# Kernel optimization log

Measured on AMD Instinct MI355X. Metric: run time of the kernel, lower is better.

Reference implementation:

```python
import jax, jax.numpy as jnp
import numpy as np

EPS = 1e-5
ABIT = 8
WBIT = 8


def ste_round(x):
    # straight-through rounding (HAWQ SymmetricQuantFunction)
    return x + jax.lax.stop_gradient(jnp.round(x) - x)


def quant_act(x, bit=ABIT):
    # per-tensor symmetric activation quantization (QuantAct)
    n = 2.0 ** (bit - 1) - 1  # 127
    scale = jnp.max(jnp.abs(x)) / n
    x_int = jnp.clip(ste_round(x / scale), -n - 1, n)
    return x_int * scale, scale


def setup_inputs() -> dict:
    key = jax.random.key(0)
    k = jax.random.split(key, 6)
    B, C_in, H, W, C_out = 32, 512, 32, 32, 128
    x = jax.random.normal(k[0], (B, C_in, H, W), jnp.float32)
    # incoming activation scale (input assumed already 8-bit quantized)
    act_scaling_factor = (jnp.max(jnp.abs(x)) / 127.0).reshape(1)
    bn_gamma = jax.random.uniform(k[1], (C_in,), jnp.float32, 0.5, 1.5)
    bn_beta = jax.random.normal(k[2], (C_in,), jnp.float32) * 0.1
    bn_mean = jax.random.normal(k[3], (C_in,), jnp.float32) * 0.1
    bn_var = jax.random.uniform(k[4], (C_in,), jnp.float32, 0.5, 1.5)
    conv_weight = jax.random.normal(k[5], (C_out, C_in, 3, 3), jnp.float32) / np.sqrt(C_in * 9)
    return {"x": x, "act_scaling_factor": act_scaling_factor,
            "bn_gamma": bn_gamma, "bn_beta": bn_beta,
            "bn_mean": bn_mean, "bn_var": bn_var,
            "conv_weight": conv_weight}


def reference(x, act_scaling_factor, bn_gamma, bn_beta, bn_mean, bn_var, conv_weight):
    nw = 2.0 ** (WBIT - 1) - 1  # 127
    s_in = act_scaling_factor.reshape(())

    # ---- QuantBn: fold BN into per-channel affine, quantize weight/bias ----
    w_bn = bn_gamma / jnp.sqrt(bn_var + EPS)            # [C_in]
    b_bn = bn_beta - bn_mean * w_bn                      # [C_in]
    ws_bn = jnp.max(jnp.abs(w_bn)) / nw                  # per-tensor weight scale
    w_int = jnp.clip(ste_round(w_bn / ws_bn), -nw - 1, nw)
    bn_sf = ws_bn * s_in                                 # bn output scaling factor
    b_int = ste_round(b_bn / bn_sf)
    x_int = x / s_in
    x = (x_int * w_int[None, :, None, None] + b_int[None, :, None, None]) * bn_sf

    # ---- ReLU ----
    x = jax.nn.relu(x)

    # ---- QuantAct: requantize activations to 8 bit ----
    x, s_act = quant_act(x)

    # ---- QuantConv2d: per-output-channel 8-bit weight quant, int conv ----
    ws_c = jnp.max(jnp.abs(conv_weight), axis=(1, 2, 3)) / nw       # [C_out]
    w_cint = jnp.clip(ste_round(conv_weight / ws_c[:, None, None, None]), -nw - 1, nw)
    y_int = jax.lax.conv_general_dilated(
        x / s_act, w_cint, window_strides=(1, 1), padding=((1, 1), (1, 1)),
        dimension_numbers=("NCHW", "OIHW", "NCHW"))
    conv_sf = s_act * ws_c                               # [C_out]
    y = y_int * conv_sf[None, :, None, None]

    # ---- QuantAct output requant ----
    y, s_out = quant_act(y)
    return (y, s_out)
```

## Files before the change

kernel.cpp:

```cpp
#include <hip/hip_runtime.h>


typedef int v4i __attribute__((ext_vector_type(4)));

#define WS_A1    64
#define WS_B1    2112
#define WS_WSC   4160
#define WS_XMX   4672
#define WS_XMN   6720
#define WS_WQ    8768
#define WS_X2    598592
#define WS_ZROW  18424384

__device__ __forceinline__ float wave_max(float m) {
#pragma unroll
    for (int off = 32; off; off >>= 1) m = fmaxf(m, __shfl_xor(m, off));
    return m;
}

__global__ __launch_bounds__(512) void k_prep(
    const float* __restrict__ gamma, const float* __restrict__ beta,
    const float* __restrict__ mean,  const float* __restrict__ var,
    const float* __restrict__ asf,   const float* __restrict__ cw,
    const float4* __restrict__ x4,
    float* ws_f, unsigned* ws_u, float* __restrict__ wsc,
    signed char* __restrict__ wq) {
    int t = threadIdx.x;
    int bid = blockIdx.x;
    __shared__ float red[16];
    if (bid < 512) {
        int c = bid;
        float mx = -3.4e38f, mn = 3.4e38f;
#pragma unroll
        for (int r = 0; r < 16; ++r) {
            int bbb = r * 2 + (t >> 8);
            float4 v = x4[((size_t)(bbb * 512 + c)) * 256 + (t & 255)];
            mx = fmaxf(mx, fmaxf(fmaxf(v.x, v.y), fmaxf(v.z, v.w)));
            mn = fminf(mn, fminf(fminf(v.x, v.y), fminf(v.z, v.w)));
        }
        mx = wave_max(mx);
        mn = -wave_max(-mn);
        if ((t & 63) == 0) { red[t >> 6] = mx; red[8 + (t >> 6)] = mn; }
        __syncthreads();
        if (t == 0) {
            float M = red[0], N = red[8];
#pragma unroll
            for (int i = 1; i < 8; ++i) { M = fmaxf(M, red[i]); N = fminf(N, red[8 + i]); }
            ws_f[WS_XMX / 4 + c] = M;
            ws_f[WS_XMN / 4 + c] = N;
        }
    } else if (bid < 640) {
        int co = bid - 512;
        const float* w = cw + (size_t)co * 4608;
        float m = 0.f;
        for (int j = t; j < 4608; j += 512) m = fmaxf(m, fabsf(w[j]));
        m = wave_max(m);
        if ((t & 63) == 0) red[t >> 6] = m;
        __syncthreads();
        float mall = red[0];
#pragma unroll
        for (int i = 1; i < 8; ++i) mall = fmaxf(mall, red[i]);
        float sc = mall / 127.0f;
        if (t == 0) wsc[co] = sc;
        int ci = t >> 6, cq = (t >> 4) & 3, cb = t & 15;
#pragma unroll
        for (int tap = 0; tap < 9; ++tap) {
            float q = fminf(fmaxf(rintf(w[t * 9 + tap] / sc), -128.f), 127.f);
            wq[(((size_t)(tap * 8 + ci) * 4 + cq) * 128 + co) * 16 + cb] = (signed char)q;
        }
    } else {
        float wbn = gamma[t] / sqrtf(var[t] + 1e-5f);
        float bbn = beta[t] - mean[t] * wbn;
        float m = wave_max(fabsf(wbn));
        if ((t & 63) == 0) red[t >> 6] = m;
        __syncthreads();
        float mall = red[0];
#pragma unroll
        for (int i = 1; i < 8; ++i) mall = fmaxf(mall, red[i]);
        float ws_bn = mall / 127.0f;
        float s_in  = asf[0];
        float bn_sf = ws_bn * s_in;
        float wint  = fminf(fmaxf(rintf(wbn / ws_bn), -128.f), 127.f);
        float bint  = rintf(bbn / bn_sf);
        ws_f[WS_A1 / 4 + t] = wint * bn_sf / s_in;
        ws_f[WS_B1 / 4 + t] = bint * bn_sf;
        if (t == 0) ws_u[1] = 0u;
    }
}

__global__ __launch_bounds__(256) void k_xquant(
    const float4* __restrict__ x4, float* __restrict__ ws_f,
    unsigned* __restrict__ x2u, unsigned* __restrict__ zrowu) {
    int bb = 31 - (blockIdx.x >> 5), h = blockIdx.x & 31;
    const float* A1 = ws_f + WS_A1 / 4;
    const float* B1 = ws_f + WS_B1 / 4;
    const float* XMX = ws_f + WS_XMX / 4;
    const float* XMN = ws_f + WS_XMN / 4;
    int t = threadIdx.x;

    __shared__ float sred[4];
    float cand = 0.f;
#pragma unroll
    for (int c0 = 0; c0 < 512; c0 += 256) {
        int c = c0 + t;
        float A = A1[c], B = B1[c];
        cand = fmaxf(cand, fmaxf(fmaf(XMX[c], A, B), fmaf(XMN[c], A, B)));
    }
    cand = wave_max(cand);
    if ((t & 63) == 0) sred[t >> 6] = cand;
    __syncthreads();
    float xm = fmaxf(fmaxf(sred[0], sred[1]), fmaxf(sred[2], sred[3]));
    float inv_sact = 127.0f / xm;
    if (blockIdx.x == 0 && t == 0) ws_f[3] = xm / 127.0f;

    size_t rowd = (size_t)(bb * 32 + h) * 4352;
    {
        int p = t >> 3, side = (t >> 2) & 1, d = t & 3;
        x2u[rowd + (p * 34 + side * 33) * 4 + d] = 0u;
    }
    if (blockIdx.x < 17) {
        int idx = blockIdx.x * 256 + t;
        if (idx < 4352) zrowu[idx] = 0u;
    }

    __shared__ unsigned lds[512 * 9];

#pragma unroll
    for (int it = 0; it < 16; ++it) {
        int idx = it * 256 + t;
        int c = idx >> 3, f4 = idx & 7;
        float4 v = x4[((size_t)bb * 512 + c) * 256 + h * 8 + f4];
        float A = A1[c] * inv_sact, B = B1[c] * inv_sact;
        unsigned q0 = (unsigned)(int)fminf(rintf(fmaxf(fmaf(v.x, A, B), 0.f)), 127.f);
        unsigned q1 = (unsigned)(int)fminf(rintf(fmaxf(fmaf(v.y, A, B), 0.f)), 127.f);
        unsigned q2 = (unsigned)(int)fminf(rintf(fmaxf(fmaf(v.z, A, B), 0.f)), 127.f);
        unsigned q3 = (unsigned)(int)fminf(rintf(fmaxf(fmaf(v.w, A, B), 0.f)), 127.f);
        lds[c * 9 + f4] = q0 | (q1 << 8) | (q2 << 16) | (q3 << 24);
    }
    __syncthreads();

#pragma unroll
    for (int it = 0; it < 4; ++it) {
        int p = it * 8 + (t >> 5);
        int s = (t >> 2) & 7;
        int k = t & 3;
        unsigned L[16];
#pragma unroll
        for (int j = 0; j < 16; ++j) L[j] = lds[(p * 16 + j) * 9 + s];
        uint4 o;
        unsigned* op = (unsigned*)&o;
#pragma unroll
        for (int d = 0; d < 4; ++d)
            op[d] = ((L[4 * d] >> (8 * k)) & 255u) |
                    (((L[4 * d + 1] >> (8 * k)) & 255u) << 8) |
                    (((L[4 * d + 2] >> (8 * k)) & 255u) << 16) |
                    (((L[4 * d + 3] >> (8 * k)) & 255u) << 24);
        *(uint4*)(x2u + rowd + (size_t)(p * 34 + s * 4 + 1 + k) * 4) = o;
    }
}

__global__ __launch_bounds__(256, 3) void k_conv(
    const unsigned char* __restrict__ x2, const unsigned char* __restrict__ zrow,
    const signed char* __restrict__ wq,
    const float* __restrict__ wsc, const float* __restrict__ ws_f,
    unsigned* __restrict__ amaxy, float* __restrict__ y) {
    __shared__ v4i red[2][1024];
    int t = threadIdx.x;
    int lane = t & 63, kv = t >> 6;
    int m = lane & 15, quad = lane >> 4;

    int bid = blockIdx.x;
    int tile = (bid & 7) * 128 + (bid >> 3);
    int ch = tile & 1;
    int rowpair = (tile >> 1) & 15;
    int bb = tile >> 5;
    int h0 = rowpair * 2;
    int co0 = ch * 64;

    const unsigned char* xb = x2 + (size_t)bb * (32 * 17408);
    const v4i* rp[4];
#pragma unroll
    for (int j = 0; j < 4; ++j) {
        int row = h0 - 1 + j;
        rp[j] = (const v4i*)(((unsigned)row < 32u) ? (xb + (size_t)row * 17408) : zrow);
    }

    v4i acc[4][4];
#pragma unroll
    for (int i = 0; i < 4; ++i)
#pragma unroll
        for (int j = 0; j < 4; ++j) acc[i][j] = (v4i){0, 0, 0, 0};

    const v4i* pw = (const v4i*)wq + quad * 128 + co0 + m;
    int abase = quad * 34 + m;

#pragma unroll
    for (int kh = 0; kh < 3; ++kh)
#pragma unroll
        for (int kw = 0; kw < 3; ++kw) {
            int tap = kh * 3 + kw;
#pragma unroll
            for (int cc = 0; cc < 2; ++cc) {
                int ci = kv * 2 + cc;
                v4i a[4];
#pragma unroll
                for (int mt = 0; mt < 4; ++mt)
                    a[mt] = rp[kh + (mt >> 1)][ci * 136 + abase + kw + (mt & 1) * 16];
#pragma unroll
                for (int nt = 0; nt < 4; ++nt) {
                    v4i bf = pw[(tap * 8 + ci) * 512 + nt * 16];
#pragma unroll
                    for (int mt = 0; mt < 4; ++mt)
                        acc[mt][nt] = __builtin_amdgcn_mfma_i32_16x16x64_i8(a[mt], bf, acc[mt][nt], 0, 0, 0);
                }
            }
        }

    if (kv >= 2) {
#pragma unroll
        for (int mt = 0; mt < 4; ++mt)
#pragma unroll
            for (int nt = 0; nt < 4; ++nt)
                red[kv - 2][(mt * 4 + nt) * 64 + lane] = acc[mt][nt];
    }
    __syncthreads();
    if (kv < 2) {
#pragma unroll
        for (int mt = 0; mt < 4; ++mt)
#pragma unroll
            for (int nt = 0; nt < 4; ++nt) {
                v4i p = red[kv][(mt * 4 + nt) * 64 + lane];
                acc[mt][nt].x += p.x; acc[mt][nt].y += p.y;
                acc[mt][nt].z += p.z; acc[mt][nt].w += p.w;
            }
    }
    __syncthreads();
    if (kv == 1) {
#pragma unroll
        for (int mt = 0; mt < 4; ++mt)
#pragma unroll
            for (int nt = 0; nt < 4; ++nt)
                red[0][(mt * 4 + nt) * 64 + lane] = acc[mt][nt];
    }
    __syncthreads();
    if (kv == 0) {
#pragma unroll
        for (int mt = 0; mt < 4; ++mt)
#pragma unroll
            for (int nt = 0; nt < 4; ++nt) {
                v4i p = red[0][(mt * 4 + nt) * 64 + lane];
                acc[mt][nt].x += p.x; acc[mt][nt].y += p.y;
                acc[mt][nt].z += p.z; acc[mt][nt].w += p.w;
            }

        float s_act = ws_f[3];
        float mx = 0.f;
#pragma unroll
        for (int nt = 0; nt < 4; ++nt) {
            int co = co0 + nt * 16 + m;
            float sf = s_act * wsc[co];
#pragma unroll
            for (int mt = 0; mt < 4; ++mt) {
                int row = h0 + (mt >> 1);
                float* yb = y + ((size_t)(bb * 128 + co)) * 1024 + row * 32 + (mt & 1) * 16;
                float4 vv;
                vv.x = (float)acc[mt][nt][0] * sf;
                vv.y = (float)acc[mt][nt][1] * sf;
                vv.z = (float)acc[mt][nt][2] * sf;
                vv.w = (float)acc[mt][nt][3] * sf;
                *(float4*)(yb + quad * 4) = vv;
                mx = fmaxf(mx, fmaxf(fmaxf(fabsf(vv.x), fabsf(vv.y)),
                                     fmaxf(fabsf(vv.z), fabsf(vv.w))));
            }
        }
        mx = wave_max(mx);
        if (lane == 0) atomicMax(amaxy, __float_as_uint(mx));
    }
}

__global__ __launch_bounds__(256) void k_yquant(float* __restrict__ yout,
                                                const unsigned* __restrict__ ws_u) {
    float s_out = __uint_as_float(ws_u[1]) / 127.0f;
    float4* y4 = (float4*)yout;
    int stride = gridDim.x * blockDim.x;
    for (int i = blockIdx.x * blockDim.x + threadIdx.x; i < 1048576; i += stride) {
        float4 v = y4[i];
        v.x = fminf(fmaxf(rintf(v.x / s_out), -128.f), 127.f) * s_out;
        v.y = fminf(fmaxf(rintf(v.y / s_out), -128.f), 127.f) * s_out;
        v.z = fminf(fmaxf(rintf(v.z / s_out), -128.f), 127.f) * s_out;
        v.w = fminf(fmaxf(rintf(v.w / s_out), -128.f), 127.f) * s_out;
        y4[i] = v;
    }
    if (blockIdx.x == 0 && threadIdx.x == 0) yout[4194304] = s_out;
}

extern "C" void kernel_launch(void* const* d_in, const int* in_sizes, int n_in,
                              void* d_out, int out_size, void* d_ws, size_t ws_size,
                              hipStream_t stream) {
    const float* x     = (const float*)d_in[0];
    const float* asf   = (const float*)d_in[1];
    const float* gamma = (const float*)d_in[2];
    const float* beta  = (const float*)d_in[3];
    const float* mean  = (const float*)d_in[4];
    const float* var   = (const float*)d_in[5];
    const float* cw    = (const float*)d_in[6];

    float*    ws_f = (float*)d_ws;
    unsigned* ws_u = (unsigned*)d_ws;
    signed char*   wq   = (signed char*)d_ws + WS_WQ;
    unsigned char* x2   = (unsigned char*)d_ws + WS_X2;
    unsigned char* zrow = (unsigned char*)d_ws + WS_ZROW;
    float* y = (float*)d_out;

    k_prep<<<641, 512, 0, stream>>>(gamma, beta, mean, var, asf, cw,
                                    (const float4*)x, ws_f, ws_u,
                                    ws_f + WS_WSC / 4, wq);
    k_xquant<<<1024, 256, 0, stream>>>((const float4*)x, ws_f,
                                       (unsigned*)x2, (unsigned*)zrow);
    k_conv<<<1024, 256, 0, stream>>>(x2, zrow, wq, ws_f + WS_WSC / 4,
                                     ws_f, ws_u + 1, y);
    k_yquant<<<1024, 256, 0, stream>>>(y, ws_u);
}
```

Baseline: 164.9 us.

## Stage conv weights in LDS and share them across two row-pairs per block

The conv kernel now covers four output rows per block (two row-pair waves pairs) with a two-way K split instead of one row-pair with a four-way split. Int8 weights for each channel chunk are staged into a 72KB LDS buffer with global_load_lds, so both row-pairs reuse them. The aim is fewer redundant global weight loads and a shorter cross-wave reduction. In exchange it adds barriers per chunk, halves the grid to 512 blocks and drops the occupancy hint from 3 to 2 blocks per CU.

```diff
diff --git a/kernel.cpp b/kernel.cpp
--- a/kernel.cpp
+++ b/kernel.cpp
@@ -16,6 +16,16 @@
 #pragma unroll
     for (int off = 32; off; off >>= 1) m = fmaxf(m, __shfl_xor(m, off));
     return m;
+}
+
+__device__ __forceinline__ void stage16(const char* g, char* s, int lane) {
+#if defined(__has_builtin) && __has_builtin(__builtin_amdgcn_global_load_lds)
+    __builtin_amdgcn_global_load_lds(
+        (const __attribute__((address_space(1))) void*)g,
+        (__attribute__((address_space(3))) void*)s, 16, 0, 0);
+#else
+    *(v4i*)(s + lane * 16) = *(const v4i*)g;
+#endif
 }
 
 __global__ __launch_bounds__(512) void k_prep(
@@ -159,30 +169,31 @@
     }
 }
 
-__global__ __launch_bounds__(256, 3) void k_conv(
+__global__ __launch_bounds__(256, 2) void k_conv(
     const unsigned char* __restrict__ x2, const unsigned char* __restrict__ zrow,
     const signed char* __restrict__ wq,
     const float* __restrict__ wsc, const float* __restrict__ ws_f,
     unsigned* __restrict__ amaxy, float* __restrict__ y) {
-    __shared__ v4i red[2][1024];
+    __shared__ char ldsb[73728];
     int t = threadIdx.x;
-    int lane = t & 63, kv = t >> 6;
+    int lane = t & 63, wv = t >> 6;
+    int kv = wv & 1, rp = wv >> 1;
     int m = lane & 15, quad = lane >> 4;
 
     int bid = blockIdx.x;
-    int tile = (bid & 7) * 128 + (bid >> 3);
+    int tile = (bid & 7) * 64 + (bid >> 3);
     int ch = tile & 1;
-    int rowpair = (tile >> 1) & 15;
-    int bb = tile >> 5;
-    int h0 = rowpair * 2;
+    int rg = (tile >> 1) & 7;
+    int bb = tile >> 4;
     int co0 = ch * 64;
+    int h0 = rg * 4 + rp * 2;
 
     const unsigned char* xb = x2 + (size_t)bb * (32 * 17408);
-    const v4i* rp[4];
+    const v4i* rpt[4];
 #pragma unroll
     for (int j = 0; j < 4; ++j) {
         int row = h0 - 1 + j;
-        rp[j] = (const v4i*)(((unsigned)row < 32u) ? (xb + (size_t)row * 17408) : zrow);
+        rpt[j] = (const v4i*)(((unsigned)row < 32u) ? (xb + (size_t)row * 17408) : zrow);
     }
 
     v4i acc[4][4];
@@ -191,56 +202,52 @@
 #pragma unroll
         for (int j = 0; j < 4; ++j) acc[i][j] = (v4i){0, 0, 0, 0};
 
-    const v4i* pw = (const v4i*)wq + quad * 128 + co0 + m;
     int abase = quad * 34 + m;
 
-#pragma unroll
-    for (int kh = 0; kh < 3; ++kh)
-#pragma unroll
-        for (int kw = 0; kw < 3; ++kw) {
-            int tap = kh * 3 + kw;
-#pragma unroll
-            for (int cc = 0; cc < 2; ++cc) {
-                int ci = kv * 2 + cc;
+    for (int j = 0; j < 4; ++j) {
+#pragma unroll
+        for (int i = 0; i < 18; ++i) {
+            int c = wv * 18 + i;
+            int kvs = (c >= 36) ? 1 : 0;
+            int rem = c - kvs * 36;
+            int tap = rem >> 2, cq = rem & 3;
+            int ci = kvs * 4 + j;
+            const char* g = (const char*)wq +
+                ((((size_t)(tap * 8 + ci) * 4 + cq) * 128 + co0) * 16) + lane * 16;
+            char* s = ldsb + (((kvs * 9 + tap) * 4 + cq) << 10);
+            stage16(g, s, lane);
+        }
+        __syncthreads();
+
+        int ci = kv * 4 + j;
+        const v4i* bbase = (const v4i*)ldsb + kv * 2304;
+#pragma unroll
+        for (int kh = 0; kh < 3; ++kh)
+#pragma unroll
+            for (int kw = 0; kw < 3; ++kw) {
+                int tap = kh * 3 + kw;
                 v4i a[4];
 #pragma unroll
                 for (int mt = 0; mt < 4; ++mt)
-                    a[mt] = rp[kh + (mt >> 1)][ci * 136 + abase + kw + (mt & 1) * 16];
+                    a[mt] = rpt[kh + (mt >> 1)][ci * 136 + abase + kw + (mt & 1) * 16];
 #pragma unroll
                 for (int nt = 0; nt < 4; ++nt) {
-                    v4i bf = pw[(tap * 8 + ci) * 512 + nt * 16];
+                    v4i bf = bbase[(tap * 4 + quad) * 64 + nt * 16 + m];
 #pragma unroll
                     for (int mt = 0; mt < 4; ++mt)
                         acc[mt][nt] = __builtin_amdgcn_mfma_i32_16x16x64_i8(a[mt], bf, acc[mt][nt], 0, 0, 0);
                 }
             }
-        }
-
-    if (kv >= 2) {
+        __syncthreads();
+    }
+
+    v4i* red = (v4i*)ldsb;
+    if (kv == 1) {
 #pragma unroll
         for (int mt = 0; mt < 4; ++mt)
 #pragma unroll
             for (int nt = 0; nt < 4; ++nt)
-                red[kv - 2][(mt * 4 + nt) * 64 + lane] = acc[mt][nt];
-    }
-    __syncthreads();
-    if (kv < 2) {
-#pragma unroll
-        for (int mt = 0; mt < 4; ++mt)
-#pragma unroll
-            for (int nt = 0; nt < 4; ++nt) {
-                v4i p = red[kv][(mt * 4 + nt) * 64 + lane];
-                acc[mt][nt].x += p.x; acc[mt][nt].y += p.y;
-                acc[mt][nt].z += p.z; acc[mt][nt].w += p.w;
-            }
-    }
-    __syncthreads();
-    if (kv == 1) {
-#pragma unroll
-        for (int mt = 0; mt < 4; ++mt)
-#pragma unroll
-            for (int nt = 0; nt < 4; ++nt)
-                red[0][(mt * 4 + nt) * 64 + lane] = acc[mt][nt];
+                red[((rp * 16 + mt * 4 + nt) << 6) + lane] = acc[mt][nt];
     }
     __syncthreads();
     if (kv == 0) {
@@ -248,7 +255,7 @@
         for (int mt = 0; mt < 4; ++mt)
 #pragma unroll
             for (int nt = 0; nt < 4; ++nt) {
-                v4i p = red[0][(mt * 4 + nt) * 64 + lane];
+                v4i p = red[((rp * 16 + mt * 4 + nt) << 6) + lane];
                 acc[mt][nt].x += p.x; acc[mt][nt].y += p.y;
                 acc[mt][nt].z += p.z; acc[mt][nt].w += p.w;
             }
@@ -317,7 +324,7 @@
                                     ws_f + WS_WSC / 4, wq);
     k_xquant<<<1024, 256, 0, stream>>>((const float4*)x, ws_f,
                                        (unsigned*)x2, (unsigned*)zrow);
-    k_conv<<<1024, 256, 0, stream>>>(x2, zrow, wq, ws_f + WS_WSC / 4,
-                                     ws_f, ws_u + 1, y);
+    k_conv<<<512, 256, 0, stream>>>(x2, zrow, wq, ws_f + WS_WSC / 4,
+                                    ws_f, ws_u + 1, y);
     k_yquant<<<1024, 256, 0, stream>>>(y, ws_u);
 }
```

After: 160.2 us. 2.9% less time.
